# Performance work log

Measured on AMD Instinct MI355X. Metric: run time of the kernel, lower is better.

## Reference

```python
import jax, jax.numpy as jnp
import numpy as np

NEG = -1000000000.0  # mask fill value from the original code


def setup_inputs() -> dict:
    key = jax.random.key(0)
    k1, k2, k3 = jax.random.split(key, 3)
    B, L, H, E = 2, 2048, 16, 64
    S, D = L, E
    queries = jax.random.normal(k1, (B, L, H, E), dtype=jnp.float32)
    keys = jax.random.normal(k2, (B, S, H, E), dtype=jnp.float32)
    values = jax.random.normal(k3, (B, S, H, D), dtype=jnp.float32)
    return {"queries": queries, "keys": keys, "values": values}


def reference(queries, keys, values):
    B, L, H, E = queries.shape
    S = keys.shape[1]
    scale = 1.0 / np.sqrt(E)
    # scores: [B, H, L, S]
    scores = jnp.einsum('blhe,bshe->bhls', queries, keys)
    # Faithful to original: tf.where(band_part(ones,-1,0), -1e9, scores)
    # i.e. fill -1e9 where the LOWER triangle (incl. diagonal) is True.
    tril = jnp.tril(jnp.ones((L, S), dtype=bool))  # [L, S]
    scores = jnp.where(tril[None, None, :, :], jnp.float32(NEG), scores)
    # scale applied AFTER masking, as in the original
    A = jax.nn.softmax(scale * scores, axis=-1)
    # dropout is identity at inference
    V = jnp.einsum('bhls,bshd->blhd', A, values)
    return V
```

## Files before the change

kernel.cpp:

```cpp
#include <hip/hip_runtime.h>


#define B_ 2
#define L_ 2048
#define H_ 16
#define E_ 64
#define S_ 2048
#define D_ 64
#define NR_ 16
#define CSH 16.0f
#define QSCALE 0.18033688011112042f

typedef __attribute__((ext_vector_type(4))) float f32x4;
typedef __attribute__((ext_vector_type(16))) float f32x16;
typedef __attribute__((ext_vector_type(8))) short short8;
typedef __attribute__((ext_vector_type(2))) unsigned int uint2v;
typedef __attribute__((ext_vector_type(4))) unsigned int uint4v;
typedef unsigned short ushort;

__device__ __forceinline__ unsigned short f2bf(float f) {
  unsigned int u = __builtin_bit_cast(unsigned int, f);
  u = (u + 0x7FFFu + ((u >> 16) & 1u)) >> 16;
  return (unsigned short)u;
}
__device__ __forceinline__ unsigned int pkbf(float a, float b) {
  return (unsigned int)f2bf(a) | ((unsigned int)f2bf(b) << 16);
}
__device__ __forceinline__ unsigned cvtpk(float a, float b) {
  unsigned r;
  asm("v_cvt_pk_bf16_f32 %0, %1, %2" : "=v"(r) : "v"(a), "v"(b));
  return r;
}
__device__ __forceinline__ uint2v plswap(unsigned a, unsigned b, int hi) {
#if __has_builtin(__builtin_amdgcn_permlane32_swap)
  (void)hi;
  return __builtin_amdgcn_permlane32_swap(a, b, false, false);
#else
  unsigned ax = (unsigned)__shfl_xor((int)a, 32);
  unsigned bx = (unsigned)__shfl_xor((int)b, 32);
  uint2v r;
  r[0] = hi ? bx : a;
  r[1] = hi ? b : ax;
  return r;
#endif
}
__device__ __forceinline__ f32x16 zero16() {
  f32x16 z;
#pragma unroll
  for (int i = 0; i < 16; ++i) z[i] = 0.f;
  return z;
}

__global__ __launch_bounds__(256) void prep_all(const float* __restrict__ Kg,
                                                const float* __restrict__ Vg,
                                                ushort* __restrict__ Kb,
                                                ushort* __restrict__ Vt,
                                                float* __restrict__ part) {
  __shared__ ushort Tl[64][72];
  const int blk = (int)blockIdx.x;
  const int tid = (int)threadIdx.x;
  if (blk < 2048) {
    const int t = blk * 256 + tid;
    const int orow = t >> 3, e0 = (t & 7) << 3;
    const int s = orow & (S_ - 1), bh = orow >> 11;
    const int b = bh >> 4, h = bh & 15;
    const float* src = Kg + ((size_t)((b * S_ + s) * H_ + h)) * E_ + e0;
    f32x4 a = ((const f32x4*)src)[0], c = ((const f32x4*)src)[1];
    short8 o;
    o[0]=(short)f2bf(a[0]); o[1]=(short)f2bf(a[1]); o[2]=(short)f2bf(a[2]); o[3]=(short)f2bf(a[3]);
    o[4]=(short)f2bf(c[0]); o[5]=(short)f2bf(c[1]); o[6]=(short)f2bf(c[2]); o[7]=(short)f2bf(c[3]);
    *(short8*)(Kb + (size_t)orow * E_ + e0) = o;
  } else {
    const int vb = blk - 2048;
    const int bh = vb & 31, st = vb >> 5;
    const int b = bh >> 4, h = bh & 15;
    const int s0 = st << 6;
    {
      const int sr = tid >> 2, d0 = (tid & 3) << 4;
      const float* src = Vg + ((size_t)((b * S_ + s0 + sr) * H_ + h)) * D_ + d0;
      f32x4 v0 = ((const f32x4*)src)[0], v1 = ((const f32x4*)src)[1];
      f32x4 v2 = ((const f32x4*)src)[2], v3 = ((const f32x4*)src)[3];
      ushort* dst = &Tl[sr][d0];
      dst[0]=f2bf(v0[0]); dst[1]=f2bf(v0[1]); dst[2]=f2bf(v0[2]); dst[3]=f2bf(v0[3]);
      dst[4]=f2bf(v1[0]); dst[5]=f2bf(v1[1]); dst[6]=f2bf(v1[2]); dst[7]=f2bf(v1[3]);
      dst[8]=f2bf(v2[0]); dst[9]=f2bf(v2[1]); dst[10]=f2bf(v2[2]); dst[11]=f2bf(v2[3]);
      dst[12]=f2bf(v3[0]); dst[13]=f2bf(v3[1]); dst[14]=f2bf(v3[2]); dst[15]=f2bf(v3[3]);
    }
    __syncthreads();
    {
      const int d = tid >> 2, sb = (tid & 3) << 4;
      short8 o0, o1;
#pragma unroll
      for (int j = 0; j < 8; ++j) {
        o0[j] = (short)Tl[sb + j][d];
        o1[j] = (short)Tl[sb + 8 + j][d];
      }
      ushort* dst = Vt + ((size_t)bh * D_ + d) * S_ + s0 + sb;
      *(short8*)dst = o0;
      *(short8*)(dst + 8) = o1;
    }
    if (tid < 64) {
      float sum = 0.f;
#pragma unroll 8
      for (int s = 0; s < 64; ++s)
        sum += __builtin_bit_cast(float, (unsigned)Tl[s][tid] << 16);
      part[(size_t)(bh * 32 + st) * 64 + tid] = sum;
    }
  }
}

struct Stage8 { short8 k[4]; short8 v[4]; };

__device__ __forceinline__ Stage8 sload(const ushort* __restrict__ Kbh,
                                        const ushort* __restrict__ VbhT,
                                        int s0, int tid) {
  Stage8 r;
  const int sl = tid >> 1, gb = (tid & 1) * 4;
  const ushort* kp = Kbh + (size_t)(s0 + sl) * E_ + gb * 8;
  r.k[0] = *(const short8*)(kp);
  r.k[1] = *(const short8*)(kp + 8);
  r.k[2] = *(const short8*)(kp + 16);
  r.k[3] = *(const short8*)(kp + 24);
  const int d = tid >> 2, sb = (tid & 3) * 32;
  const ushort* vp = VbhT + (size_t)d * S_ + s0 + sb;
  r.v[0] = *(const short8*)(vp);
  r.v[1] = *(const short8*)(vp + 8);
  r.v[2] = *(const short8*)(vp + 16);
  r.v[3] = *(const short8*)(vp + 24);
  return r;
}

__device__ __forceinline__ void swrite(ushort* SM, const Stage8& r, int tid) {
  const int sl = tid >> 1, gb = (tid & 1) * 4;
#pragma unroll
  for (int j = 0; j < 4; ++j)
    *(short8*)(SM + sl * 64 + (((gb + j) ^ (sl & 7)) << 3)) = r.k[j];
  const int d = tid >> 2, sgb = (tid & 3) * 4;
#pragma unroll
  for (int j = 0; j < 4; ++j) {
    const int sgg = sgb + j;
    *(short8*)(SM + 8192 + (sgg >> 3) * 4096 + d * 64 + (((sgg & 7) ^ (d & 7)) << 3)) = r.v[j];
  }
}

__global__ __launch_bounds__(256, 2) void attn_fwd17(
    const float* __restrict__ Qg, const ushort* __restrict__ Kb,
    const ushort* __restrict__ Vt, float* __restrict__ Og) {
  const int bh = (int)blockIdx.x;
  const int b = bh >> 4, h = bh & 15;
  const int yi0 = (int)blockIdx.y;
  const int yi = (yi0 < 8) ? yi0 : 23 - yi0;
  const int q0 = yi << 7;
  const int tid = (int)threadIdx.x;
  const int w = tid >> 6, lane = tid & 63;
  const int hi = lane >> 5, c32 = lane & 31;
  const int qbase = q0 + (w << 5);
  const int qrow = qbase + c32;

  __shared__ __align__(16) ushort SM[2][16384];

  const ushort* Kbh = Kb + (size_t)bh * (S_ * E_);
  const ushort* VbhT = Vt + (size_t)bh * (D_ * S_);

  short8 qf[4];
  {
    const float* qr = Qg + ((size_t)((b * L_ + qrow) * H_ + h)) * E_;
#pragma unroll
    for (int kc = 0; kc < 4; ++kc) {
      f32x4 x = *(const f32x4*)(qr + kc * 16 + hi * 8);
      f32x4 y = *(const f32x4*)(qr + kc * 16 + hi * 8 + 4);
      short8 q;
      q[0]=(short)f2bf(QSCALE*x[0]); q[1]=(short)f2bf(QSCALE*x[1]);
      q[2]=(short)f2bf(QSCALE*x[2]); q[3]=(short)f2bf(QSCALE*x[3]);
      q[4]=(short)f2bf(QSCALE*y[0]); q[5]=(short)f2bf(QSCALE*y[1]);
      q[6]=(short)f2bf(QSCALE*y[2]); q[7]=(short)f2bf(QSCALE*y[3]);
      qf[kc] = q;
    }
  }

  f32x16 acc0 = zero16(), acc1 = zero16();
  float dsum = 0.f;

  const int r0 = (q0 + 1) >> 7;

  {
    Stage8 s = sload(Kbh, VbhT, r0 << 7, tid);
    swrite(SM[0], s, tid);
  }
  __syncthreads();

  for (int r = r0; r < NR_; ++r) {
    const int cur = (r - r0) & 1;
    const bool more = (r + 1) < NR_;
    Stage8 nxt;
    if (more) nxt = sload(Kbh, VbhT, (r + 1) << 7, tid);

    const ushort* img = SM[cur];
#pragma unroll
    for (int half = 0; half < 2; ++half) {
      const int s0 = (r << 7) + (half << 6);
      if (s0 + 63 > qbase) {
        f32x16 st0 = zero16(), st1 = zero16();
        __builtin_amdgcn_s_setprio(1);
#pragma unroll
        for (int kc = 0; kc < 4; ++kc) {
          const int gg = 2 * kc + hi;
          const int rl0 = (half << 6) + c32, rl1 = rl0 + 32;
          short8 k0 = *(const short8*)(img + rl0 * 64 + ((gg ^ (rl0 & 7)) << 3));
          short8 k1 = *(const short8*)(img + rl1 * 64 + ((gg ^ (rl1 & 7)) << 3));
          st0 = __builtin_amdgcn_mfma_f32_32x32x16_bf16(k0, qf[kc], st0, 0, 0, 0);
          st1 = __builtin_amdgcn_mfma_f32_32x32x16_bf16(k1, qf[kc], st1, 0, 0, 0);
        }
        __builtin_amdgcn_s_setprio(0);

        if (s0 < qbase + 32) {
#pragma unroll
          for (int r16 = 0; r16 < 16; ++r16) {
            const int ko = (r16 & 3) + 8 * (r16 >> 2) + 4 * hi;
            st0[r16] = (s0 + ko <= qrow) ? -1e30f : st0[r16];
            st1[r16] = (s0 + 32 + ko <= qrow) ? -1e30f : st1[r16];
          }
        }

        float ps = 0.f;
#pragma unroll
        for (int r16 = 0; r16 < 16; ++r16) { st0[r16] = exp2f(st0[r16] - CSH); ps += st0[r16]; }
#pragma unroll
        for (int r16 = 0; r16 < 16; ++r16) { st1[r16] = exp2f(st1[r16] - CSH); ps += st1[r16]; }
        dsum += ps;

        short8 pf[4];
#pragma unroll
        for (int kp = 0; kp < 4; ++kp) {
          const f32x16 stt = (kp < 2) ? st0 : st1;
          const int u = kp & 1;
          unsigned pA0 = cvtpk(stt[8 * u + 0], stt[8 * u + 1]);
          unsigned pA1 = cvtpk(stt[8 * u + 2], stt[8 * u + 3]);
          unsigned pB0 = cvtpk(stt[8 * u + 4], stt[8 * u + 5]);
          unsigned pB1 = cvtpk(stt[8 * u + 6], stt[8 * u + 7]);
          uint2v sw0 = plswap(pA0, pB0, hi);
          uint2v sw1 = plswap(pA1, pB1, hi);
          uint4v fv;
          fv[0] = sw0[0]; fv[1] = sw1[0]; fv[2] = sw0[1]; fv[3] = sw1[1];
          pf[kp] = __builtin_bit_cast(short8, fv);
        }

        __builtin_amdgcn_s_setprio(1);
#pragma unroll
        for (int kp = 0; kp < 4; ++kp) {
          const int sg = 2 * kp + hi;
          const ushort* vb = img + 8192 + half * 4096;
          short8 v0 = *(const short8*)(vb + c32 * 64 + ((sg ^ (c32 & 7)) << 3));
          short8 v1 = *(const short8*)(vb + (32 + c32) * 64 + ((sg ^ (c32 & 7)) << 3));
          acc0 = __builtin_amdgcn_mfma_f32_32x32x16_bf16(pf[kp], v0, acc0, 0, 0, 0);
          acc1 = __builtin_amdgcn_mfma_f32_32x32x16_bf16(pf[kp], v1, acc1, 0, 0, 0);
        }
        __builtin_amdgcn_s_setprio(0);
      }
    }

    if (more) swrite(SM[cur ^ 1], nxt, tid);
    __syncthreads();
  }

  float dfull = dsum + __shfl_xor(dsum, 32);
#pragma unroll
  for (int r16 = 0; r16 < 16; ++r16) {
    const int row = (r16 & 3) + 8 * (r16 >> 2) + 4 * hi;
    const float dn = __shfl(dfull, row);
    const int grow = qbase + row;
    if (grow != L_ - 1) {
      const float inv = 1.0f / dn;
      const size_t base = ((size_t)((b * L_ + grow) * H_ + h)) * D_;
      Og[base + c32] = acc0[r16] * inv;
      Og[base + 32 + c32] = acc1[r16] * inv;
    }
  }
}

__global__ __launch_bounds__(64) void vmean_comb(const float* __restrict__ part,
                                                 float* __restrict__ Og) {
  const int bh = blockIdx.x;
  const int b = bh >> 4, h = bh & 15;
  const int lane = (int)threadIdx.x;
  float t = 0.f;
#pragma unroll
  for (int i = 0; i < 32; ++i) t += part[(size_t)(bh * 32 + i) * 64 + lane];
  Og[((size_t)((b * L_ + (L_ - 1)) * H_ + h)) * D_ + lane] = t * (1.0f / (float)S_);
}

__global__ __launch_bounds__(256) void attn_fwd(
    const float* __restrict__ Qg, const float* __restrict__ Kg,
    const float* __restrict__ Vg, float* __restrict__ Og) {
  const int bh = blockIdx.x;
  const int b = bh >> 4, h = bh & 15;
  const int q0 = blockIdx.y << 6;
  const int tid = (int)threadIdx.x;
  const int lane = tid & 63;
  const int w = tid >> 6;
  const int gp = lane >> 4;
  const int c = lane & 15;
  const int qbase = q0 + (w << 4);

  __shared__ unsigned short Kl[32][72];
  __shared__ unsigned short Vts[64][40];

  short8 qf0, qf1;
  {
    const float* qrow = Qg + ((size_t)((b * L_ + (qbase + c)) * H_ + h)) * E_;
    const f32x4* q0p = (const f32x4*)(qrow + (gp << 3));
    const f32x4* q1p = (const f32x4*)(qrow + 32 + (gp << 3));
    f32x4 a0 = q0p[0], b0 = q0p[1], a1 = q1p[0], b1 = q1p[1];
    float t0[8] = {a0[0],a0[1],a0[2],a0[3],b0[0],b0[1],b0[2],b0[3]};
    float t1[8] = {a1[0],a1[1],a1[2],a1[3],b1[0],b1[1],b1[2],b1[3]};
#pragma unroll
    for (int j = 0; j < 8; ++j) {
      qf0[j] = (short)f2bf(0.125f * t0[j]);
      qf1[j] = (short)f2bf(0.125f * t1[j]);
    }
  }

  f32x4 accO[4];
#pragma unroll
  for (int k0 = 0; k0 < 4; ++k0) accO[k0] = (f32x4){0.f, 0.f, 0.f, 0.f};
  float m_run = -1e30f, denom = 0.f;

  const int c0 = (q0 + 1) >> 5;
  const int srow = tid >> 3;
  const int scol = (tid & 7) << 3;

  for (int ch = c0; ch < (S_ >> 5); ++ch) {
    const int s0 = ch << 5;
    __syncthreads();
    {
      const size_t rbase = ((size_t)((b * S_ + (s0 + srow)) * H_ + h));
      const float* kp = Kg + rbase * E_ + scol;
      f32x4 ka = *(const f32x4*)kp;
      f32x4 kb = *(const f32x4*)(kp + 4);
      short8 kv;
      kv[0]=(short)f2bf(ka[0]); kv[1]=(short)f2bf(ka[1]);
      kv[2]=(short)f2bf(ka[2]); kv[3]=(short)f2bf(ka[3]);
      kv[4]=(short)f2bf(kb[0]); kv[5]=(short)f2bf(kb[1]);
      kv[6]=(short)f2bf(kb[2]); kv[7]=(short)f2bf(kb[3]);
      *(short8*)&Kl[srow][scol] = kv;
      const float* vp = Vg + rbase * D_ + scol;
      f32x4 va = *(const f32x4*)vp;
      f32x4 vb = *(const f32x4*)(vp + 4);
      Vts[scol + 0][srow] = f2bf(va[0]);
      Vts[scol + 1][srow] = f2bf(va[1]);
      Vts[scol + 2][srow] = f2bf(va[2]);
      Vts[scol + 3][srow] = f2bf(va[3]);
      Vts[scol + 4][srow] = f2bf(vb[0]);
      Vts[scol + 5][srow] = f2bf(vb[1]);
      Vts[scol + 6][srow] = f2bf(vb[2]);
      Vts[scol + 7][srow] = f2bf(vb[3]);
    }
    __syncthreads();
    if (s0 + 31 <= qbase) continue;

    f32x4 st0 = {0.f,0.f,0.f,0.f}, st1 = {0.f,0.f,0.f,0.f};
    {
      short8 kf;
      kf = *(const short8*)&Kl[c][(gp << 3)];
      st0 = __builtin_amdgcn_mfma_f32_16x16x32_bf16(kf, qf0, st0, 0, 0, 0);
      kf = *(const short8*)&Kl[c][32 + (gp << 3)];
      st0 = __builtin_amdgcn_mfma_f32_16x16x32_bf16(kf, qf1, st0, 0, 0, 0);
      kf = *(const short8*)&Kl[16 + c][(gp << 3)];
      st1 = __builtin_amdgcn_mfma_f32_16x16x32_bf16(kf, qf0, st1, 0, 0, 0);
      kf = *(const short8*)&Kl[16 + c][32 + (gp << 3)];
      st1 = __builtin_amdgcn_mfma_f32_16x16x32_bf16(kf, qf1, st1, 0, 0, 0);
    }

    const int lrow = qbase + c;
    float p[8];
    {
      float sarr[8] = {st0[0], st0[1], st0[2], st0[3], st1[0], st1[1], st1[2], st1[3]};
      float mx = -1e30f;
#pragma unroll
      for (int i = 0; i < 8; ++i) {
        int sg = s0 + ((i >> 2) << 4) + (gp << 2) + (i & 3);
        float v = (sg > lrow) ? sarr[i] : -1e30f;
        p[i] = v;
        mx = fmaxf(mx, v);
      }
      mx = fmaxf(mx, __shfl_xor(mx, 16));
      mx = fmaxf(mx, __shfl_xor(mx, 32));
      float m_new = fmaxf(m_run, mx);
      float sum = 0.f;
#pragma unroll
      for (int i = 0; i < 8; ++i) { p[i] = __expf(p[i] - m_new); sum += p[i]; }
      sum += __shfl_xor(sum, 16);
      sum += __shfl_xor(sum, 32);
      float alpha = __expf(m_run - m_new);
      m_run = m_new;
      denom = denom * alpha + sum;
      float ar0 = __shfl(alpha, (gp << 2) + 0);
      float ar1 = __shfl(alpha, (gp << 2) + 1);
      float ar2 = __shfl(alpha, (gp << 2) + 2);
      float ar3 = __shfl(alpha, (gp << 2) + 3);
#pragma unroll
      for (int k0 = 0; k0 < 4; ++k0) {
        accO[k0][0] *= ar0; accO[k0][1] *= ar1;
        accO[k0][2] *= ar2; accO[k0][3] *= ar3;
      }
    }

    {
      unsigned int pA0 = pkbf(p[0], p[1]), pA1 = pkbf(p[2], p[3]);
      unsigned int pB0 = pkbf(p[4], p[5]), pB1 = pkbf(p[6], p[7]);
      const int al = (gp << 1) & 3;
      const int src0 = (al << 4) + c, src1 = src0 + 16;
      unsigned int a0 = (unsigned int)__shfl((int)pA0, src0);
      unsigned int a1 = (unsigned int)__shfl((int)pA1, src0);
      unsigned int a2 = (unsigned int)__shfl((int)pA0, src1);
      unsigned int a3 = (unsigned int)__shfl((int)pA1, src1);
      unsigned int b0 = (unsigned int)__shfl((int)pB0, src0);
      unsigned int b1 = (unsigned int)__shfl((int)pB1, src0);
      unsigned int b2 = (unsigned int)__shfl((int)pB0, src1);
      unsigned int b3 = (unsigned int)__shfl((int)pB1, src1);
      const bool useA = (gp < 2);
      uint4v fv;
      fv[0] = useA ? a0 : b0;
      fv[1] = useA ? a1 : b1;
      fv[2] = useA ? a2 : b2;
      fv[3] = useA ? a3 : b3;
      short8 pfv = __builtin_bit_cast(short8, fv);
#pragma unroll
      for (int k0 = 0; k0 < 4; ++k0) {
        short8 vf = *(const short8*)&Vts[(k0 << 4) + c][(gp << 3)];
        accO[k0] = __builtin_amdgcn_mfma_f32_16x16x32_bf16(pfv, vf, accO[k0], 0, 0, 0);
      }
    }
  }

  float dr[4];
  dr[0] = __shfl(denom, (gp << 2) + 0);
  dr[1] = __shfl(denom, (gp << 2) + 1);
  dr[2] = __shfl(denom, (gp << 2) + 2);
  dr[3] = __shfl(denom, (gp << 2) + 3);
#pragma unroll
  for (int r = 0; r < 4; ++r) {
    const int grow = qbase + (gp << 2) + r;
    if (grow == L_ - 1) continue;
    const size_t base = ((size_t)((b * L_ + grow) * H_ + h)) * D_ + c;
    const float inv = 1.0f / dr[r];
    Og[base +  0] = accO[0][r] * inv;
    Og[base + 16] = accO[1][r] * inv;
    Og[base + 32] = accO[2][r] * inv;
    Og[base + 48] = accO[3][r] * inv;
  }
}

__global__ __launch_bounds__(256) void vmean_fix(const float* __restrict__ Vg,
                                                 float* __restrict__ Og) {
  const int bh = blockIdx.x;
  const int b = bh >> 4, h = bh & 15;
  const int t = (int)threadIdx.x;
  const int lane = t & 63, w = t >> 6;
  float sum = 0.f;
  for (int s = w; s < S_; s += 4)
    sum += Vg[((size_t)((b * S_ + s) * H_ + h)) * D_ + lane];
  __shared__ float red[4][64];
  red[w][lane] = sum;
  __syncthreads();
  if (w == 0) {
    float tot = red[0][lane] + red[1][lane] + red[2][lane] + red[3][lane];
    Og[((size_t)((b * L_ + (L_ - 1)) * H_ + h)) * D_ + lane] = tot * (1.0f / (float)S_);
  }
}

extern "C" void kernel_launch(void* const* d_in, const int* in_sizes, int n_in,
                              void* d_out, int out_size, void* d_ws, size_t ws_size,
                              hipStream_t stream) {
  const float* Q = (const float*)d_in[0];
  const float* K = (const float*)d_in[1];
  const float* V = (const float*)d_in[2];
  float* O = (float*)d_out;
  const size_t szK = (size_t)B_ * H_ * S_ * E_ * 2;
  const size_t szV = (size_t)B_ * H_ * D_ * S_ * 2;
  const size_t szP = (size_t)(B_ * H_ * 32) * 64 * 4;

  if (ws_size >= szK + szV + szP) {
    ushort* Kb = (ushort*)d_ws;
    ushort* Vt = (ushort*)((char*)d_ws + szK);
    float* part = (float*)((char*)d_ws + szK + szV);
    prep_all<<<dim3(3072), dim3(256), 0, stream>>>(K, V, Kb, Vt, part);
    attn_fwd17<<<dim3(B_ * H_, L_ / 128), dim3(256), 0, stream>>>(Q, Kb, Vt, O);
    vmean_comb<<<dim3(B_ * H_), dim3(64), 0, stream>>>(part, O);
  } else {
    attn_fwd<<<dim3(B_ * H_, L_ / 64), dim3(256), 0, stream>>>(Q, K, V, O);
    vmean_fix<<<dim3(B_ * H_), dim3(256), 0, stream>>>(V, O);
  }
}
```

Before: 61.21 us.

## Shrink attention blocks to 64 query rows with 64-key stages and new grid mapping

Moves the main attention kernel from 256-thread blocks covering 128 query rows over a 2D grid to 128-thread blocks covering 64 query rows, launched as a flat 1024-block grid. Each block now stages 64 keys per pipeline step, so the shared-memory tile halves. Block IDs are remapped so consecutive blocks share a query tile across 32 batch-heads, and the old pairing of short and long causal rows is dropped. The aim is finer load balancing across the triangular work and more resident blocks per CU. The cost is twice as many loop iterations and barriers per key range, plus less reuse of each staged K/V tile.

```diff
diff --git a/kernel.cpp b/kernel.cpp
--- a/kernel.cpp
+++ b/kernel.cpp
@@ -7,7 +7,7 @@
 #define E_ 64
 #define S_ 2048
 #define D_ 64
-#define NR_ 16
+#define NR_ 32
 #define CSH 16.0f
 #define QSCALE 0.18033688011112042f
 
@@ -109,19 +109,19 @@
   }
 }
 
-struct Stage8 { short8 k[4]; short8 v[4]; };
-
-__device__ __forceinline__ Stage8 sload(const ushort* __restrict__ Kbh,
-                                        const ushort* __restrict__ VbhT,
-                                        int s0, int tid) {
-  Stage8 r;
+struct Stage18 { short8 k[4]; short8 v[4]; };
+
+__device__ __forceinline__ Stage18 sload(const ushort* __restrict__ Kbh,
+                                         const ushort* __restrict__ VbhT,
+                                         int s0, int tid) {
+  Stage18 r;
   const int sl = tid >> 1, gb = (tid & 1) * 4;
   const ushort* kp = Kbh + (size_t)(s0 + sl) * E_ + gb * 8;
   r.k[0] = *(const short8*)(kp);
   r.k[1] = *(const short8*)(kp + 8);
   r.k[2] = *(const short8*)(kp + 16);
   r.k[3] = *(const short8*)(kp + 24);
-  const int d = tid >> 2, sb = (tid & 3) * 32;
+  const int d = tid >> 1, sb = (tid & 1) * 32;
   const ushort* vp = VbhT + (size_t)d * S_ + s0 + sb;
   r.v[0] = *(const short8*)(vp);
   r.v[1] = *(const short8*)(vp + 8);
@@ -130,34 +130,34 @@
   return r;
 }
 
-__device__ __forceinline__ void swrite(ushort* SM, const Stage8& r, int tid) {
+__device__ __forceinline__ void swrite(ushort* SM, const Stage18& r, int tid) {
   const int sl = tid >> 1, gb = (tid & 1) * 4;
 #pragma unroll
   for (int j = 0; j < 4; ++j)
     *(short8*)(SM + sl * 64 + (((gb + j) ^ (sl & 7)) << 3)) = r.k[j];
-  const int d = tid >> 2, sgb = (tid & 3) * 4;
+  const int d = tid >> 1, sgb = (tid & 1) * 4;
 #pragma unroll
   for (int j = 0; j < 4; ++j) {
-    const int sgg = sgb + j;
-    *(short8*)(SM + 8192 + (sgg >> 3) * 4096 + d * 64 + (((sgg & 7) ^ (d & 7)) << 3)) = r.v[j];
-  }
-}
-
-__global__ __launch_bounds__(256, 2) void attn_fwd17(
+    const int sg = sgb + j;
+    *(short8*)(SM + 4096 + d * 64 + ((sg ^ (d & 7)) << 3)) = r.v[j];
+  }
+}
+
+__global__ __launch_bounds__(128, 2) void attn_fwd18(
     const float* __restrict__ Qg, const ushort* __restrict__ Kb,
     const ushort* __restrict__ Vt, float* __restrict__ Og) {
-  const int bh = (int)blockIdx.x;
+  const int bid = (int)blockIdx.x;
+  const int bh = (bid & 7) + 8 * ((bid >> 3) & 3);
+  const int yi = bid >> 5;
   const int b = bh >> 4, h = bh & 15;
-  const int yi0 = (int)blockIdx.y;
-  const int yi = (yi0 < 8) ? yi0 : 23 - yi0;
-  const int q0 = yi << 7;
+  const int q0 = yi << 6;
   const int tid = (int)threadIdx.x;
   const int w = tid >> 6, lane = tid & 63;
   const int hi = lane >> 5, c32 = lane & 31;
   const int qbase = q0 + (w << 5);
   const int qrow = qbase + c32;
 
-  __shared__ __align__(16) ushort SM[2][16384];
+  __shared__ __align__(16) ushort SM[2][8192];
 
   const ushort* Kbh = Kb + (size_t)bh * (S_ * E_);
   const ushort* VbhT = Vt + (size_t)bh * (D_ * S_);
@@ -181,10 +181,10 @@
   f32x16 acc0 = zero16(), acc1 = zero16();
   float dsum = 0.f;
 
-  const int r0 = (q0 + 1) >> 7;
+  const int r0 = (q0 + 1) >> 6;
 
   {
-    Stage8 s = sload(Kbh, VbhT, r0 << 7, tid);
+    Stage18 s = sload(Kbh, VbhT, r0 << 6, tid);
     swrite(SM[0], s, tid);
   }
   __syncthreads();
@@ -192,71 +192,68 @@
   for (int r = r0; r < NR_; ++r) {
     const int cur = (r - r0) & 1;
     const bool more = (r + 1) < NR_;
-    Stage8 nxt;
-    if (more) nxt = sload(Kbh, VbhT, (r + 1) << 7, tid);
+    Stage18 nxt;
+    if (more) nxt = sload(Kbh, VbhT, (r + 1) << 6, tid);
 
     const ushort* img = SM[cur];
-#pragma unroll
-    for (int half = 0; half < 2; ++half) {
-      const int s0 = (r << 7) + (half << 6);
-      if (s0 + 63 > qbase) {
-        f32x16 st0 = zero16(), st1 = zero16();
-        __builtin_amdgcn_s_setprio(1);
-#pragma unroll
-        for (int kc = 0; kc < 4; ++kc) {
-          const int gg = 2 * kc + hi;
-          const int rl0 = (half << 6) + c32, rl1 = rl0 + 32;
-          short8 k0 = *(const short8*)(img + rl0 * 64 + ((gg ^ (rl0 & 7)) << 3));
-          short8 k1 = *(const short8*)(img + rl1 * 64 + ((gg ^ (rl1 & 7)) << 3));
-          st0 = __builtin_amdgcn_mfma_f32_32x32x16_bf16(k0, qf[kc], st0, 0, 0, 0);
-          st1 = __builtin_amdgcn_mfma_f32_32x32x16_bf16(k1, qf[kc], st1, 0, 0, 0);
+    const int s0 = r << 6;
+    if (s0 + 63 > qbase) {
+      f32x16 st0 = zero16(), st1 = zero16();
+      __builtin_amdgcn_s_setprio(1);
+#pragma unroll
+      for (int kc = 0; kc < 4; ++kc) {
+        const int gg = 2 * kc + hi;
+        const int rl0 = c32, rl1 = c32 + 32;
+        short8 k0 = *(const short8*)(img + rl0 * 64 + ((gg ^ (rl0 & 7)) << 3));
+        short8 k1 = *(const short8*)(img + rl1 * 64 + ((gg ^ (rl1 & 7)) << 3));
+        st0 = __builtin_amdgcn_mfma_f32_32x32x16_bf16(k0, qf[kc], st0, 0, 0, 0);
+        st1 = __builtin_amdgcn_mfma_f32_32x32x16_bf16(k1, qf[kc], st1, 0, 0, 0);
+      }
+      __builtin_amdgcn_s_setprio(0);
+
+      if (s0 < qbase + 32) {
+#pragma unroll
+        for (int r16 = 0; r16 < 16; ++r16) {
+          const int ko = (r16 & 3) + 8 * (r16 >> 2) + 4 * hi;
+          st0[r16] = (s0 + ko <= qrow) ? -1e30f : st0[r16];
+          st1[r16] = (s0 + 32 + ko <= qrow) ? -1e30f : st1[r16];
         }
-        __builtin_amdgcn_s_setprio(0);
-
-        if (s0 < qbase + 32) {
-#pragma unroll
-          for (int r16 = 0; r16 < 16; ++r16) {
-            const int ko = (r16 & 3) + 8 * (r16 >> 2) + 4 * hi;
-            st0[r16] = (s0 + ko <= qrow) ? -1e30f : st0[r16];
-            st1[r16] = (s0 + 32 + ko <= qrow) ? -1e30f : st1[r16];
-          }
-        }
-
-        float ps = 0.f;
-#pragma unroll
-        for (int r16 = 0; r16 < 16; ++r16) { st0[r16] = exp2f(st0[r16] - CSH); ps += st0[r16]; }
-#pragma unroll
-        for (int r16 = 0; r16 < 16; ++r16) { st1[r16] = exp2f(st1[r16] - CSH); ps += st1[r16]; }
-        dsum += ps;
-
-        short8 pf[4];
-#pragma unroll
-        for (int kp = 0; kp < 4; ++kp) {
-          const f32x16 stt = (kp < 2) ? st0 : st1;
-          const int u = kp & 1;
-          unsigned pA0 = cvtpk(stt[8 * u + 0], stt[8 * u + 1]);
-          unsigned pA1 = cvtpk(stt[8 * u + 2], stt[8 * u + 3]);
-          unsigned pB0 = cvtpk(stt[8 * u + 4], stt[8 * u + 5]);
-          unsigned pB1 = cvtpk(stt[8 * u + 6], stt[8 * u + 7]);
-          uint2v sw0 = plswap(pA0, pB0, hi);
-          uint2v sw1 = plswap(pA1, pB1, hi);
-          uint4v fv;
-          fv[0] = sw0[0]; fv[1] = sw1[0]; fv[2] = sw0[1]; fv[3] = sw1[1];
-          pf[kp] = __builtin_bit_cast(short8, fv);
-        }
-
-        __builtin_amdgcn_s_setprio(1);
-#pragma unroll
-        for (int kp = 0; kp < 4; ++kp) {
-          const int sg = 2 * kp + hi;
-          const ushort* vb = img + 8192 + half * 4096;
-          short8 v0 = *(const short8*)(vb + c32 * 64 + ((sg ^ (c32 & 7)) << 3));
-          short8 v1 = *(const short8*)(vb + (32 + c32) * 64 + ((sg ^ (c32 & 7)) << 3));
-          acc0 = __builtin_amdgcn_mfma_f32_32x32x16_bf16(pf[kp], v0, acc0, 0, 0, 0);
-          acc1 = __builtin_amdgcn_mfma_f32_32x32x16_bf16(pf[kp], v1, acc1, 0, 0, 0);
-        }
-        __builtin_amdgcn_s_setprio(0);
-      }
+      }
+
+      float ps = 0.f;
+#pragma unroll
+      for (int r16 = 0; r16 < 16; ++r16) { st0[r16] = exp2f(st0[r16] - CSH); ps += st0[r16]; }
+#pragma unroll
+      for (int r16 = 0; r16 < 16; ++r16) { st1[r16] = exp2f(st1[r16] - CSH); ps += st1[r16]; }
+      dsum += ps;
+
+      short8 pf[4];
+#pragma unroll
+      for (int kp = 0; kp < 4; ++kp) {
+        const f32x16 stt = (kp < 2) ? st0 : st1;
+        const int u = kp & 1;
+        unsigned pA0 = cvtpk(stt[8 * u + 0], stt[8 * u + 1]);
+        unsigned pA1 = cvtpk(stt[8 * u + 2], stt[8 * u + 3]);
+        unsigned pB0 = cvtpk(stt[8 * u + 4], stt[8 * u + 5]);
+        unsigned pB1 = cvtpk(stt[8 * u + 6], stt[8 * u + 7]);
+        uint2v sw0 = plswap(pA0, pB0, hi);
+        uint2v sw1 = plswap(pA1, pB1, hi);
+        uint4v fv;
+        fv[0] = sw0[0]; fv[1] = sw1[0]; fv[2] = sw0[1]; fv[3] = sw1[1];
+        pf[kp] = __builtin_bit_cast(short8, fv);
+      }
+
+      __builtin_amdgcn_s_setprio(1);
+#pragma unroll
+      for (int kp = 0; kp < 4; ++kp) {
+        const int sg = 2 * kp + hi;
+        const ushort* vb = img + 4096;
+        short8 v0 = *(const short8*)(vb + c32 * 64 + ((sg ^ (c32 & 7)) << 3));
+        short8 v1 = *(const short8*)(vb + (32 + c32) * 64 + ((sg ^ (c32 & 7)) << 3));
+        acc0 = __builtin_amdgcn_mfma_f32_32x32x16_bf16(pf[kp], v0, acc0, 0, 0, 0);
+        acc1 = __builtin_amdgcn_mfma_f32_32x32x16_bf16(pf[kp], v1, acc1, 0, 0, 0);
+      }
+      __builtin_amdgcn_s_setprio(0);
     }
 
     if (more) swrite(SM[cur ^ 1], nxt, tid);
@@ -485,7 +482,7 @@
     ushort* Vt = (ushort*)((char*)d_ws + szK);
     float* part = (float*)((char*)d_ws + szK + szV);
     prep_all<<<dim3(3072), dim3(256), 0, stream>>>(K, V, Kb, Vt, part);
-    attn_fwd17<<<dim3(B_ * H_, L_ / 128), dim3(256), 0, stream>>>(Q, Kb, Vt, O);
+    attn_fwd18<<<dim3(1024), dim3(128), 0, stream>>>(Q, Kb, Vt, O);
     vmean_comb<<<dim3(B_ * H_), dim3(64), 0, stream>>>(part, O);
   } else {
     attn_fwd<<<dim3(B_ * H_, L_ / 64), dim3(256), 0, stream>>>(Q, K, V, O);
```

New measurement: 72.77 us. 1.19x slower.

## Split long-row query tiles across two blocks and merge partial results

Applied to the files above, without the earlier changes.

The heavy query tiles (first 8 of 16, which see the most unmasked keys) are split into two blocks, each covering half of the key range. The partial numerators and denominators go to workspace and a new merge kernel combines them. The point is to balance work across the 768 blocks and shorten the critical path, since the old version paired heavy and light tiles within a block's y index. The cost is an extra kernel launch, global writes and reads of the partial accumulators, and a larger workspace requirement.

```diff
diff --git a/kernel.cpp b/kernel.cpp
--- a/kernel.cpp
+++ b/kernel.cpp
@@ -143,21 +143,16 @@
   }
 }
 
-__global__ __launch_bounds__(256, 2) void attn_fwd17(
+__device__ __forceinline__ void tile_body(
     const float* __restrict__ Qg, const ushort* __restrict__ Kb,
-    const ushort* __restrict__ Vt, float* __restrict__ Og) {
-  const int bh = (int)blockIdx.x;
-  const int b = bh >> 4, h = bh & 15;
-  const int yi0 = (int)blockIdx.y;
-  const int yi = (yi0 < 8) ? yi0 : 23 - yi0;
-  const int q0 = yi << 7;
-  const int tid = (int)threadIdx.x;
+    const ushort* __restrict__ Vt, ushort* SM0, ushort* SM1,
+    int b, int h, int bh, int q0, int rs, int re, int tid,
+    f32x16& acc0, f32x16& acc1, float& dsum, int& qbase_o, int& qrow_o) {
   const int w = tid >> 6, lane = tid & 63;
   const int hi = lane >> 5, c32 = lane & 31;
   const int qbase = q0 + (w << 5);
   const int qrow = qbase + c32;
-
-  __shared__ __align__(16) ushort SM[2][16384];
+  qbase_o = qbase; qrow_o = qrow;
 
   const ushort* Kbh = Kb + (size_t)bh * (S_ * E_);
   const ushort* VbhT = Vt + (size_t)bh * (D_ * S_);
@@ -178,24 +173,22 @@
     }
   }
 
-  f32x16 acc0 = zero16(), acc1 = zero16();
-  float dsum = 0.f;
-
-  const int r0 = (q0 + 1) >> 7;
+  acc0 = zero16(); acc1 = zero16(); dsum = 0.f;
 
   {
-    Stage8 s = sload(Kbh, VbhT, r0 << 7, tid);
-    swrite(SM[0], s, tid);
+    Stage8 s = sload(Kbh, VbhT, rs << 7, tid);
+    swrite(SM0, s, tid);
   }
   __syncthreads();
 
-  for (int r = r0; r < NR_; ++r) {
-    const int cur = (r - r0) & 1;
-    const bool more = (r + 1) < NR_;
+  for (int r = rs; r < re; ++r) {
+    ushort* SMc = ((r - rs) & 1) ? SM1 : SM0;
+    ushort* SMn = ((r - rs) & 1) ? SM0 : SM1;
+    const bool more = (r + 1) < re;
     Stage8 nxt;
     if (more) nxt = sload(Kbh, VbhT, (r + 1) << 7, tid);
 
-    const ushort* img = SM[cur];
+    const ushort* img = SMc;
 #pragma unroll
     for (int half = 0; half < 2; ++half) {
       const int s0 = (r << 7) + (half << 6);
@@ -259,9 +252,118 @@
       }
     }
 
-    if (more) swrite(SM[cur ^ 1], nxt, tid);
+    if (more) swrite(SMn, nxt, tid);
     __syncthreads();
   }
+}
+
+__global__ __launch_bounds__(256, 2) void attn_fwd19(
+    const float* __restrict__ Qg, const ushort* __restrict__ Kb,
+    const ushort* __restrict__ Vt, float* __restrict__ pacc,
+    float* __restrict__ pd, float* __restrict__ Og) {
+  const int bh = (int)blockIdx.x;
+  const int b = bh >> 4, h = bh & 15;
+  const int y = (int)blockIdx.y;
+  const int tid = (int)threadIdx.x;
+  const int w = tid >> 6, lane = tid & 63;
+  const int hi = lane >> 5, c32 = lane & 31;
+
+  __shared__ __align__(16) ushort SM[2][16384];
+
+  int yi, rs, re;
+  bool split;
+  if (y < 16) {
+    split = true;
+    yi = y >> 1;
+    const int r0 = ((yi << 7) + 1) >> 7;
+    const int R = NR_ - r0;
+    const int mid = r0 + ((R + 1) >> 1);
+    rs = (y & 1) ? mid : r0;
+    re = (y & 1) ? NR_ : mid;
+  } else {
+    split = false;
+    yi = y - 8;
+    rs = ((yi << 7) + 1) >> 7;
+    re = NR_;
+  }
+  const int q0 = yi << 7;
+
+  f32x16 acc0, acc1;
+  float dsum;
+  int qbase, qrow;
+  tile_body(Qg, Kb, Vt, SM[0], SM[1], b, h, bh, q0, rs, re, tid,
+            acc0, acc1, dsum, qbase, qrow);
+
+  if (split) {
+    const int half = y & 1;
+    const size_t tb = (size_t)((bh * 8 + yi) * 2 + half);
+    float* pa = pacc + tb * (128 * 64);
+    float dfull = dsum + __shfl_xor(dsum, 32);
+    if (hi == 0) pd[tb * 128 + (w << 5) + c32] = dfull;
+#pragma unroll
+    for (int r16 = 0; r16 < 16; ++r16) {
+      const int row = (r16 & 3) + 8 * (r16 >> 2) + 4 * hi;
+      const int ql = (w << 5) + row;
+      pa[ql * 64 + c32] = acc0[r16];
+      pa[ql * 64 + 32 + c32] = acc1[r16];
+    }
+  } else {
+    float dfull = dsum + __shfl_xor(dsum, 32);
+#pragma unroll
+    for (int r16 = 0; r16 < 16; ++r16) {
+      const int row = (r16 & 3) + 8 * (r16 >> 2) + 4 * hi;
+      const float dn = __shfl(dfull, row);
+      const int grow = qbase + row;
+      if (grow != L_ - 1) {
+        const float inv = 1.0f / dn;
+        const size_t base = ((size_t)((b * L_ + grow) * H_ + h)) * D_;
+        Og[base + c32] = acc0[r16] * inv;
+        Og[base + 32 + c32] = acc1[r16] * inv;
+      }
+    }
+  }
+}
+
+__global__ __launch_bounds__(256) void merge_split(const float* __restrict__ pacc,
+                                                   const float* __restrict__ pd,
+                                                   float* __restrict__ Og) {
+  const int bh = (int)blockIdx.x, yi = (int)blockIdx.y;
+  const int b = bh >> 4, h = bh & 15;
+  const int tid = (int)threadIdx.x;
+  const size_t t0 = (size_t)((bh * 8 + yi) * 2);
+  const float* pa = pacc + t0 * (128 * 64);
+  const float* pb = pa + 128 * 64;
+  const int q0 = yi << 7;
+#pragma unroll
+  for (int i = 0; i < 32; ++i) {
+    const int e = tid + (i << 8);
+    const int ql = e >> 6, d = e & 63;
+    const float dn = pd[t0 * 128 + ql] + pd[(t0 + 1) * 128 + ql];
+    const float num = pa[e] + pb[e];
+    Og[((size_t)((b * L_ + q0 + ql) * H_ + h)) * D_ + d] = num / dn;
+  }
+}
+
+__global__ __launch_bounds__(256, 2) void attn_fwd17(
+    const float* __restrict__ Qg, const ushort* __restrict__ Kb,
+    const ushort* __restrict__ Vt, float* __restrict__ Og) {
+  const int bh = (int)blockIdx.x;
+  const int b = bh >> 4, h = bh & 15;
+  const int yi0 = (int)blockIdx.y;
+  const int yi = (yi0 < 8) ? yi0 : 23 - yi0;
+  const int q0 = yi << 7;
+  const int tid = (int)threadIdx.x;
+  const int w = tid >> 6, lane = tid & 63;
+  const int hi = lane >> 5, c32 = lane & 31;
+
+  __shared__ __align__(16) ushort SM[2][16384];
+
+  const int rs = (q0 + 1) >> 7;
+  f32x16 acc0, acc1;
+  float dsum;
+  int qbase, qrow;
+  tile_body(Qg, Kb, Vt, SM[0], SM[1], b, h, bh, q0, rs, NR_, tid,
+            acc0, acc1, dsum, qbase, qrow);
 
   float dfull = dsum + __shfl_xor(dsum, 32);
 #pragma unroll
@@ -479,8 +581,20 @@
   const size_t szK = (size_t)B_ * H_ * S_ * E_ * 2;
   const size_t szV = (size_t)B_ * H_ * D_ * S_ * 2;
   const size_t szP = (size_t)(B_ * H_ * 32) * 64 * 4;
-
-  if (ws_size >= szK + szV + szP) {
+  const size_t szA = (size_t)32 * 8 * 2 * 128 * 64 * 4;
+  const size_t szD = (size_t)32 * 8 * 2 * 128 * 4;
+
+  if (ws_size >= szK + szV + szP + szA + szD) {
+    ushort* Kb = (ushort*)d_ws;
+    ushort* Vt = (ushort*)((char*)d_ws + szK);
+    float* part = (float*)((char*)d_ws + szK + szV);
+    float* pacc = (float*)((char*)d_ws + szK + szV + szP);
+    float* pd = (float*)((char*)d_ws + szK + szV + szP + szA);
+    prep_all<<<dim3(3072), dim3(256), 0, stream>>>(K, V, Kb, Vt, part);
+    attn_fwd19<<<dim3(32, 24), dim3(256), 0, stream>>>(Q, Kb, Vt, pacc, pd, O);
+    merge_split<<<dim3(32, 8), dim3(256), 0, stream>>>(pacc, pd, O);
+    vmean_comb<<<dim3(B_ * H_), dim3(64), 0, stream>>>(part, O);
+  } else if (ws_size >= szK + szV + szP) {
     ushort* Kb = (ushort*)d_ws;
     ushort* Vt = (ushort*)((char*)d_ws + szK);
     float* part = (float*)((char*)d_ws + szK + szV);
```

New measurement: 73.35 us. 1.2x slower.
